# Kernel optimization log

Measured on AMD Instinct MI355X. Metric: run time of the kernel, lower is better.

## Reference

```python
import jax, jax.numpy as jnp
import numpy as np

D_MODEL = 1024
N_HEADS = 16
HEAD_DIM = D_MODEL // N_HEADS
B, T = 4, 2048


def setup_inputs() -> dict:
    key = jax.random.key(0)
    ks = jax.random.split(key, 5)
    s = 1.0 / np.sqrt(D_MODEL)
    return {
        "x": jax.random.normal(ks[0], (B, T, D_MODEL), dtype=jnp.float32),
        "Wq": jax.random.normal(ks[1], (D_MODEL, D_MODEL), dtype=jnp.float32) * s,
        "bq": jnp.zeros((D_MODEL,), jnp.float32),
        "Wk": jax.random.normal(ks[2], (D_MODEL, D_MODEL), dtype=jnp.float32) * s,
        "bk": jnp.zeros((D_MODEL,), jnp.float32),
        "Wv": jax.random.normal(ks[3], (D_MODEL, D_MODEL), dtype=jnp.float32) * s,
        "bv": jnp.zeros((D_MODEL,), jnp.float32),
        "Wo": jax.random.normal(ks[4], (D_MODEL, D_MODEL), dtype=jnp.float32) * s,
        "bo": jnp.zeros((D_MODEL,), jnp.float32),
    }


def reference(x, Wq, bq, Wk, bk, Wv, bv, Wo, bo):
    Bx, Tx, C = x.shape
    H, Dh = N_HEADS, HEAD_DIM
    # projections (torch Linear: y = x @ W.T + b)
    q = (x @ Wq.T + bq).reshape(Bx, Tx, H, Dh).transpose(0, 2, 1, 3)  # [B,H,T,Dh]
    k = (x @ Wk.T + bk).reshape(Bx, Tx, H, Dh).transpose(0, 2, 1, 3)
    v = (x @ Wv.T + bv).reshape(Bx, Tx, H, Dh).transpose(0, 2, 1, 3)
    scores = jnp.einsum("bhqd,bhkd->bhqk", q, k) / np.sqrt(Dh).astype(np.float32)
    causal = jnp.tril(jnp.ones((Tx, Tx), dtype=bool))
    scores = jnp.where(causal, scores, -jnp.inf)
    attn = jax.nn.softmax(scores, axis=-1)  # dropout in eval mode = identity
    y = jnp.einsum("bhqk,bhkd->bhqd", attn, v)
    y = y.transpose(0, 2, 1, 3).reshape(Bx, Tx, C)
    return y @ Wo.T + bo
```

## Files before the change

### kernel.cpp

```cpp
#include <hip/hip_runtime.h>

typedef __attribute__((ext_vector_type(8))) short short8;
typedef __attribute__((ext_vector_type(4))) float f32x4;
typedef unsigned short u16;
typedef unsigned int u32;

#define NH 16

#if __has_builtin(__builtin_amdgcn_exp2f)
#define EXP2(x) __builtin_amdgcn_exp2f(x)
#else
#define EXP2(x) exp2f(x)
#endif

__device__ __forceinline__ u32 f2bf(float f) {
  u32 u = __builtin_bit_cast(u32, f);
  return (u + 0x7fffu + ((u >> 16) & 1u)) >> 16;
}

__device__ __forceinline__ void gload_lds16(const u16* g, u16* l) {
  __builtin_amdgcn_global_load_lds(
      (const __attribute__((address_space(1))) void*)g,
      (__attribute__((address_space(3))) void*)l, 16, 0, 0);
}

__global__ __launch_bounds__(256) void k_convert(
    const float* __restrict__ x, const float* __restrict__ wq,
    const float* __restrict__ wk, const float* __restrict__ wv,
    const float* __restrict__ wo, u16* __restrict__ dst) {
  int i = blockIdx.x * 256 + threadIdx.x;
  size_t e = (size_t)i * 4;
  const float* s; size_t off;
  if (e < 8388608ull)       { s = x;  off = e; }
  else if (e < 9437184ull)  { s = wq; off = e - 8388608ull; }
  else if (e < 10485760ull) { s = wk; off = e - 9437184ull; }
  else if (e < 11534336ull) { s = wv; off = e - 10485760ull; }
  else                      { s = wo; off = e - 11534336ull; }
  float4 d = *(const float4*)(s + off);
  ushort4 o;
  o.x = (u16)f2bf(d.x); o.y = (u16)f2bf(d.y);
  o.z = (u16)f2bf(d.z); o.w = (u16)f2bf(d.w);
  *(ushort4*)(dst + e) = o;
}

#define GPHASE(MH, NH_, LA, LB)                                                \
  if (LA) {                                                                    \
    _Pragma("unroll")                                                          \
    for (int mt = 0; mt < 4; ++mt)                                             \
      _Pragma("unroll")                                                        \
      for (int ks = 0; ks < 2; ++ks)                                           \
        af[mt][ks] = *(const short8*)(Ab +                                     \
            (wr * MT * 16 + ((MH) * 4 + mt) * 16 + l16) * 64 +                 \
            ((ks * 4 + quad) ^ swz) * 8);                                      \
  }                                                                            \
  if (LB) {                                                                    \
    _Pragma("unroll")                                                          \
    for (int nt = 0; nt < NH2; ++nt)                                           \
      _Pragma("unroll")                                                        \
      for (int ks = 0; ks < 2; ++ks)                                           \
        bfr[nt][ks] = *(const short8*)(Bb +                                    \
            (wn * NT * 16 + ((NH_) * NH2 + nt) * 16 + l16) * 64 +              \
            ((ks * 4 + quad) ^ swz) * 8);                                      \
  }                                                                            \
  __builtin_amdgcn_s_barrier();                                                \
  __builtin_amdgcn_s_setprio(1);                                               \
  _Pragma("unroll")                                                            \
  for (int mt = 0; mt < 4; ++mt)                                               \
    _Pragma("unroll")                                                          \
    for (int nt = 0; nt < NH2; ++nt)                                           \
      _Pragma("unroll")                                                        \
      for (int ks = 0; ks < 2; ++ks)                                           \
        acc[(MH) * 4 + mt][(NH_) * NH2 + nt] =                                 \
            __builtin_amdgcn_mfma_f32_16x16x32_bf16(                           \
                af[mt][ks], bfr[nt][ks], acc[(MH) * 4 + mt][(NH_) * NH2 + nt], \
                0, 0, 0);                                                      \
  __builtin_amdgcn_s_setprio(0);                                               \
  __builtin_amdgcn_s_barrier();                                                \
  __builtin_amdgcn_sched_barrier(0);

#define STAGE_T(T, PB)                                                         \
  {                                                                            \
    const u16* aT = aTh + (T) * 64;                                            \
    const u16* bT = bTh + (T) * 64;                                            \
    u16* aD = &As[PB][0] + dbase;                                              \
    u16* bD = &Bs[PB][0] + dbase;                                              \
    _Pragma("unroll")                                                          \
    for (int j = 0; j < NLA; ++j) gload_lds16(aT + j * 65536, aD + j * 4096);  \
    _Pragma("unroll")                                                          \
    for (int j = 0; j < NLB; ++j) gload_lds16(bT + j * 65536, bD + j * 4096);  \
  }

template <int MT, int NT>
__device__ __forceinline__ void gemm_core(const u16* __restrict__ Aptr,
                                          const u16* __restrict__ Bptr,
                                          int m0, int n0, f32x4 (&acc)[8][4]) {
  constexpr int NLA = MT / 2;
  constexpr int NLB = NT;
  constexpr int NLD = NLA + NLB;
  constexpr int NH2 = NT / 2;
  __shared__ u16 As[2][MT * 32 * 64];
  __shared__ u16 Bs[2][NT * 64 * 64];
  const int tid = threadIdx.x;
  const int wave = tid >> 6, lane = tid & 63;
  const int quad = lane >> 4, l16 = lane & 15;
  const int wr = wave >> 2, wn = wave & 3;
  const int swz = l16 & 7;
  const int srow = tid >> 3;
  const int srcg = (tid & 7) ^ (srow & 7);
  const u16* aTh = Aptr + (size_t)(m0 + srow) * 1024 + srcg * 8;
  const u16* bTh = Bptr + (size_t)(n0 + srow) * 1024 + srcg * 8;
  const int dbase = wave * 512;

  {
    f32x4 z = {0.f, 0.f, 0.f, 0.f};
    #pragma unroll
    for (int a = 0; a < 8; ++a)
      #pragma unroll
      for (int b2 = 0; b2 < 4; ++b2) acc[a][b2] = z;
  }

  STAGE_T(0, 0)

  short8 af[4][2], bfr[NH2][2];
  for (int t = 0; t < 16; ++t) {
    const int p = t & 1;
    if (t < 15) {
      STAGE_T(t + 1, p ^ 1)
      if constexpr (NLD == 8)
        asm volatile("s_waitcnt vmcnt(8)" ::: "memory");
      else if constexpr (NLD == 6)
        asm volatile("s_waitcnt vmcnt(6)" ::: "memory");
      else
        asm volatile("s_waitcnt vmcnt(0)" ::: "memory");
    } else {
      asm volatile("s_waitcnt vmcnt(0)" ::: "memory");
    }
    __builtin_amdgcn_s_barrier();
    __builtin_amdgcn_sched_barrier(0);
    const u16* Ab = &As[p][0];
    const u16* Bb = &Bs[p][0];
    GPHASE(0, 0, true, true)
    GPHASE(0, 1, false, true)
    GPHASE(1, 1, true, false)
    GPHASE(1, 0, false, true)
  }
}

__global__ __launch_bounds__(512, 2) void k_gemm_qkv(
    const u16* __restrict__ A, const u16* __restrict__ W,
    const float* __restrict__ bq, const float* __restrict__ bk,
    const float* __restrict__ bv, u16* __restrict__ qkv,
    u16* __restrict__ vt) {
  const int bid = blockIdx.x;
  const int sw = (bid & 7) * 48 + (bid >> 3);
  const int ntile = sw % 12, mtile = sw / 12;
  const int m0 = mtile * 256, n0 = ntile * 256;
  const int z = n0 >> 10;
  const float* bias = (z == 0) ? bq : (z == 1) ? bk : bv;
  u16* out = qkv + (size_t)z * 8388608;
  const float scl = (z == 0) ? 0.125f * 1.44269504088896340736f : 1.0f;
  f32x4 acc[8][4];
  gemm_core<8, 4>(A, W, m0, n0, acc);
  const int tid = threadIdx.x;
  const int wave = tid >> 6, lane = tid & 63;
  const int quad = lane >> 4, l16 = lane & 15;
  const int wr = wave >> 2, wn = wave & 3;
  if (z == 2) {
    #pragma unroll
    for (int mt = 0; mt < 8; ++mt) {
      #pragma unroll
      for (int nt = 0; nt < 4; ++nt) {
        int nn = (n0 + wn * 64 + nt * 16 + l16) & 1023;
        float bn = bias[nn];
        int h = nn >> 6, d = nn & 63;
        int mbase = m0 + wr * 128 + mt * 16 + quad * 4;
        int b = mbase >> 11, tb = mbase & 2047;
        uint2 pk;
        pk.x = f2bf(acc[mt][nt][0] + bn) | (f2bf(acc[mt][nt][1] + bn) << 16);
        pk.y = f2bf(acc[mt][nt][2] + bn) | (f2bf(acc[mt][nt][3] + bn) << 16);
        *(uint2*)(vt + ((size_t)(b * NH + h) * 64 + d) * 2048 + tb) = pk;
      }
    }
  } else {
    #pragma unroll
    for (int mt = 0; mt < 8; ++mt) {
      #pragma unroll
      for (int nt = 0; nt < 4; ++nt) {
        int nn = (n0 + wn * 64 + nt * 16 + l16) & 1023;
        float bn = bias[nn];
        int h = nn >> 6, d = nn & 63;
        #pragma unroll
        for (int r = 0; r < 4; ++r) {
          int m = m0 + wr * 128 + mt * 16 + quad * 4 + r;
          int b = m >> 11, tt = m & 2047;
          float val = (acc[mt][nt][r] + bn) * scl;
          out[(((size_t)(b * NH + h) * 2048 + tt) << 6) + d] = (u16)f2bf(val);
        }
      }
    }
  }
}

__global__ __launch_bounds__(512, 2) void k_gemm_out(
    const u16* __restrict__ A, const u16* __restrict__ Bw,
    const float* __restrict__ bias, float* __restrict__ out) {
  const int bid = blockIdx.x;
  const int sw = (bid & 7) * 32 + (bid >> 3);
  const int mtile = sw >> 3, ntile = sw & 7;
  const int m0 = mtile * 256, n0 = ntile * 128;
  f32x4 acc[8][4];
  gemm_core<8, 2>(A, Bw, m0, n0, acc);
  const int tid = threadIdx.x;
  const int wave = tid >> 6, lane = tid & 63;
  const int quad = lane >> 4, l16 = lane & 15;
  const int wr = wave >> 2, wn = wave & 3;
  #pragma unroll
  for (int mt = 0; mt < 8; ++mt) {
    #pragma unroll
    for (int nt = 0; nt < 2; ++nt) {
      int n = n0 + wn * 32 + nt * 16 + l16;
      float bn = bias[n];
      #pragma unroll
      for (int r = 0; r < 4; ++r) {
        int m = m0 + wr * 128 + mt * 16 + quad * 4 + r;
        out[(size_t)m * 1024 + n] = acc[mt][nt][r] + bn;
      }
    }
  }
}

#define ATTN_SUB(P, QF0, QF1, O, MI, LI, DIAG)                                 \
  {                                                                            \
    f32x4 st[4];                                                               \
    _Pragma("unroll")                                                          \
    for (int nt = 0; nt < 4; ++nt) {                                           \
      short8 kf0 = *(const short8*)(&Ks[P][(nt * 16 + l16) * 72 + quad * 8]);  \
      short8 kf1 = *(const short8*)(&Ks[P][(nt * 16 + l16) * 72 + 32 + quad * 8]); \
      f32x4 z4 = {0.f, 0.f, 0.f, 0.f};                                         \
      z4 = __builtin_amdgcn_mfma_f32_16x16x32_bf16(kf0, QF0, z4, 0, 0, 0);     \
      st[nt] = __builtin_amdgcn_mfma_f32_16x16x32_bf16(kf1, QF1, z4, 0, 0, 0); \
    }                                                                          \
    if (DIAG) {                                                                \
      int q_loc = wave * 16 + l16;                                             \
      _Pragma("unroll")                                                        \
      for (int nt = 0; nt < 4; ++nt) {                                         \
        _Pragma("unroll")                                                      \
        for (int r = 0; r < 4; ++r) {                                          \
          int k_loc = nt * 16 + quad * 4 + r;                                  \
          if (k_loc > q_loc) st[nt][r] = -1e30f;                               \
        }                                                                      \
      }                                                                        \
    }                                                                          \
    float mq[4];                                                               \
    _Pragma("unroll")                                                          \
    for (int nt = 0; nt < 4; ++nt)                                             \
      mq[nt] = fmaxf(fmaxf(st[nt][0], st[nt][1]), fmaxf(st[nt][2], st[nt][3]));\
    float mx = fmaxf(fmaxf(mq[0], mq[1]), fmaxf(mq[2], mq[3]));                \
    mx = fmaxf(mx, __shfl_xor(mx, 16, 64));                                    \
    mx = fmaxf(mx, __shfl_xor(mx, 32, 64));                                    \
    float mnew = fmaxf(MI, mx);                                                \
    float alpha = EXP2(MI - mnew);                                             \
    MI = mnew;                                                                 \
    LI *= alpha;                                                               \
    _Pragma("unroll")                                                          \
    for (int r = 0; r < 4; ++r) {                                              \
      float av = __shfl(alpha, quad * 4 + r, 16);                              \
      _Pragma("unroll")                                                        \
      for (int dt = 0; dt < 4; ++dt) O[dt][r] *= av;                           \
    }                                                                          \
    u32 Wx[4], Wy[4];                                                          \
    float sq[4];                                                               \
    _Pragma("unroll")                                                          \
    for (int nt = 0; nt < 4; ++nt) {                                           \
      float p0 = EXP2(st[nt][0] - mnew);                                       \
      float p1 = EXP2(st[nt][1] - mnew);                                       \
      float p2 = EXP2(st[nt][2] - mnew);                                       \
      float p3 = EXP2(st[nt][3] - mnew);                                       \
      sq[nt] = (p0 + p1) + (p2 + p3);                                          \
      Wx[nt] = f2bf(p0) | (f2bf(p1) << 16);                                    \
      Wy[nt] = f2bf(p2) | (f2bf(p3) << 16);                                    \
    }                                                                          \
    float sum = (sq[0] + sq[1]) + (sq[2] + sq[3]);                             \
    sum += __shfl_xor(sum, 16, 64);                                            \
    sum += __shfl_xor(sum, 32, 64);                                            \
    LI += sum;                                                                 \
    uint4 t0, t1;                                                              \
    {                                                                          \
      u32 e, f;                                                                \
      e = __shfl(Wx[0], s0, 64); f = __shfl(Wx[1], s0, 64); t0.x = hi ? f : e; \
      e = __shfl(Wy[0], s0, 64); f = __shfl(Wy[1], s0, 64); t0.y = hi ? f : e; \
      e = __shfl(Wx[0], s1, 64); f = __shfl(Wx[1], s1, 64); t0.z = hi ? f : e; \
      e = __shfl(Wy[0], s1, 64); f = __shfl(Wy[1], s1, 64); t0.w = hi ? f : e; \
      e = __shfl(Wx[2], s0, 64); f = __shfl(Wx[3], s0, 64); t1.x = hi ? f : e; \
      e = __shfl(Wy[2], s0, 64); f = __shfl(Wy[3], s0, 64); t1.y = hi ? f : e; \
      e = __shfl(Wx[2], s1, 64); f = __shfl(Wx[3], s1, 64); t1.z = hi ? f : e; \
      e = __shfl(Wy[2], s1, 64); f = __shfl(Wy[3], s1, 64); t1.w = hi ? f : e; \
    }                                                                          \
    short8 pf0 = __builtin_bit_cast(short8, t0);                               \
    short8 pf1 = __builtin_bit_cast(short8, t1);                               \
    _Pragma("unroll")                                                          \
    for (int dt = 0; dt < 4; ++dt) {                                           \
      short8 vf0 = *(const short8*)(&Vs[P][(dt * 16 + l16) * 72 + quad * 8]);  \
      short8 vf1 = *(const short8*)(&Vs[P][(dt * 16 + l16) * 72 + 32 + quad * 8]); \
      O[dt] = __builtin_amdgcn_mfma_f32_16x16x32_bf16(pf0, vf0, O[dt], 0, 0, 0); \
      O[dt] = __builtin_amdgcn_mfma_f32_16x16x32_bf16(pf1, vf1, O[dt], 0, 0, 0); \
    }                                                                          \
  }

#define ATTN_EPI(O, LI, QT)                                                    \
  _Pragma("unroll")                                                            \
  for (int r = 0; r < 4; ++r) {                                                \
    float lv = __shfl(LI, quad * 4 + r, 16);                                   \
    float inv = 1.0f / lv;                                                     \
    int t = (QT) * 64 + wave * 16 + quad * 4 + r;                              \
    _Pragma("unroll")                                                          \
    for (int dt = 0; dt < 4; ++dt) {                                           \
      int d = dt * 16 + l16;                                                   \
      y[(((size_t)b * 2048 + t) * NH + h) * 64 + d] = (u16)f2bf(O[dt][r] * inv); \
    }                                                                          \
  }

__global__ __launch_bounds__(256, 4) void k_attn(
    const u16* __restrict__ q, const u16* __restrict__ k,
    const u16* __restrict__ vt, u16* __restrict__ y) {
  const int tid = threadIdx.x;
  const int wave = tid >> 6, lane = tid & 63;
  const int quad = lane >> 4, l16 = lane & 15;
  const int bh = blockIdx.x, bx = blockIdx.y;
  const int qtB = bx, qtA = 31 - bx;
  const int b = bh >> 4, h = bh & 15;

  __shared__ u16 Ks[2][64 * 72];
  __shared__ u16 Vs[2][64 * 72];

  const u16* qbA = q + ((size_t)bh * 2048 + qtA * 64 + wave * 16 + l16) * 64;
  short8 qA0 = *(const short8*)(qbA + quad * 8);
  short8 qA1 = *(const short8*)(qbA + 32 + quad * 8);
  const u16* qbB = q + ((size_t)bh * 2048 + qtB * 64 + wave * 16 + l16) * 64;
  short8 qB0 = *(const short8*)(qbB + quad * 8);
  short8 qB1 = *(const short8*)(qbB + 32 + quad * 8);

  f32x4 oA[4], oB[4];
  {
    f32x4 z = {0.f, 0.f, 0.f, 0.f};
    #pragma unroll
    for (int dt = 0; dt < 4; ++dt) { oA[dt] = z; oB[dt] = z; }
  }
  float mA = -1e30f, lA = 0.f, mB = -1e30f, lB = 0.f;

  const u16* kbase = k + (size_t)bh * 131072;
  const u16* vbase = vt + (size_t)bh * 131072;
  const int r0 = tid >> 3, cc = tid & 7;
  const int s0 = ((quad & 1) << 5) + l16, s1 = s0 + 16;
  const int hi = quad >> 1;

  {
    uint4 k0 = *(const uint4*)(kbase + (size_t)r0 * 64 + cc * 8);
    uint4 k1 = *(const uint4*)(kbase + (size_t)(r0 + 32) * 64 + cc * 8);
    uint4 v0 = *(const uint4*)(vbase + (size_t)r0 * 2048 + cc * 8);
    uint4 v1 = *(const uint4*)(vbase + (size_t)(r0 + 32) * 2048 + cc * 8);
    *(uint4*)(&Ks[0][r0 * 72 + cc * 8]) = k0;
    *(uint4*)(&Ks[0][(r0 + 32) * 72 + cc * 8]) = k1;
    *(uint4*)(&Vs[0][r0 * 72 + cc * 8]) = v0;
    *(uint4*)(&Vs[0][(r0 + 32) * 72 + cc * 8]) = v1;
  }
  __syncthreads();

  for (int kt = 0; kt <= qtA; ++kt) {
    const int p = kt & 1;
    const bool pre = (kt < qtA);
    uint4 kr0, kr1, vr0, vr1;
    if (pre) {
      const u16* kb = kbase + (size_t)(kt + 1) * 4096;
      const u16* vb = vbase + (kt + 1) * 64;
      kr0 = *(const uint4*)(kb + (size_t)r0 * 64 + cc * 8);
      kr1 = *(const uint4*)(kb + (size_t)(r0 + 32) * 64 + cc * 8);
      vr0 = *(const uint4*)(vb + (size_t)r0 * 2048 + cc * 8);
      vr1 = *(const uint4*)(vb + (size_t)(r0 + 32) * 2048 + cc * 8);
    }

    ATTN_SUB(p, qA0, qA1, oA, mA, lA, (kt == qtA))
    if (kt <= qtB) {
      ATTN_SUB(p, qB0, qB1, oB, mB, lB, (kt == qtB))
    }

    if (pre) {
      *(uint4*)(&Ks[p ^ 1][r0 * 72 + cc * 8]) = kr0;
      *(uint4*)(&Ks[p ^ 1][(r0 + 32) * 72 + cc * 8]) = kr1;
      *(uint4*)(&Vs[p ^ 1][r0 * 72 + cc * 8]) = vr0;
      *(uint4*)(&Vs[p ^ 1][(r0 + 32) * 72 + cc * 8]) = vr1;
    }
    __syncthreads();
  }

  ATTN_EPI(oA, lA, qtA)
  ATTN_EPI(oB, lB, qtB)
}

extern "C" void kernel_launch(void* const* d_in, const int* in_sizes, int n_in,
                              void* d_out, int out_size, void* d_ws, size_t ws_size,
                              hipStream_t stream) {
  const float* x  = (const float*)d_in[0];
  const float* Wq = (const float*)d_in[1];
  const float* bq = (const float*)d_in[2];
  const float* Wk = (const float*)d_in[3];
  const float* bk = (const float*)d_in[4];
  const float* Wv = (const float*)d_in[5];
  const float* bv = (const float*)d_in[6];
  const float* Wo = (const float*)d_in[7];
  const float* bo = (const float*)d_in[8];
  float* out = (float*)d_out;

  u16* ws  = (u16*)d_ws;
  u16* xb  = ws;
  u16* Wb  = ws + 8388608;
  u16* qkv = ws + 12582912;
  u16* vt  = ws + 37748736;
  u16* y   = ws + 46137344;

  k_convert<<<dim3(12288), dim3(256), 0, stream>>>(x, Wq, Wk, Wv, Wo, ws);
  k_gemm_qkv<<<dim3(384), dim3(512), 0, stream>>>(xb, Wb, bq, bk, bv, qkv, vt);
  k_attn<<<dim3(64, 16), dim3(256), 0, stream>>>(qkv, qkv + 8388608, vt, y);
  k_gemm_out<<<dim3(256), dim3(512), 0, stream>>>(y, Wb + 3 * 1048576, bo, out);
}
```

Baseline: 301.6 us.

## Halve QKV GEMM M-tile and use hardware packed bf16 conversion

The QKV projection GEMM now uses 128x256 tiles with 768 blocks instead of 256x256 with 384, so the grid covers the 256 CUs more evenly. The gemm core is generalized to the tile shape, with a matching vmcnt wait and a shortened phase sequence. Separately, software float-to-bf16 rounding in the convert, epilogue and attention softmax paths is replaced by the v_cvt_pk_bf16_f32 instruction. Smaller tiles lower data reuse and raise global and LDS traffic per flop. The hardware conversion may also differ slightly from the manual rounding on NaN handling.

```diff
diff --git a/kernel.cpp b/kernel.cpp
--- a/kernel.cpp
+++ b/kernel.cpp
@@ -16,6 +16,12 @@
 __device__ __forceinline__ u32 f2bf(float f) {
   u32 u = __builtin_bit_cast(u32, f);
   return (u + 0x7fffu + ((u >> 16) & 1u)) >> 16;
+}
+
+__device__ __forceinline__ u32 cvtpk(float lo, float hi) {
+  u32 r;
+  asm("v_cvt_pk_bf16_f32 %0, %1, %2" : "=v"(r) : "v"(lo), "v"(hi));
+  return r;
 }
 
 __device__ __forceinline__ void gload_lds16(const u16* g, u16* l) {
@@ -37,10 +43,10 @@
   else if (e < 11534336ull) { s = wv; off = e - 10485760ull; }
   else                      { s = wo; off = e - 11534336ull; }
   float4 d = *(const float4*)(s + off);
-  ushort4 o;
-  o.x = (u16)f2bf(d.x); o.y = (u16)f2bf(d.y);
-  o.z = (u16)f2bf(d.z); o.w = (u16)f2bf(d.w);
-  *(ushort4*)(dst + e) = o;
+  uint2 o;
+  o.x = cvtpk(d.x, d.y);
+  o.y = cvtpk(d.z, d.w);
+  *(uint2*)(dst + e) = o;
 }
 
 #define GPHASE(MH, NH_, LA, LB)                                                \
@@ -93,7 +99,8 @@
 template <int MT, int NT>
 __device__ __forceinline__ void gemm_core(const u16* __restrict__ Aptr,
                                           const u16* __restrict__ Bptr,
-                                          int m0, int n0, f32x4 (&acc)[8][4]) {
+                                          int m0, int n0,
+                                          f32x4 (&acc)[MT][NT]) {
   constexpr int NLA = MT / 2;
   constexpr int NLB = NT;
   constexpr int NLD = NLA + NLB;
@@ -114,9 +121,9 @@
   {
     f32x4 z = {0.f, 0.f, 0.f, 0.f};
     #pragma unroll
-    for (int a = 0; a < 8; ++a)
+    for (int a = 0; a < MT; ++a)
       #pragma unroll
-      for (int b2 = 0; b2 < 4; ++b2) acc[a][b2] = z;
+      for (int b2 = 0; b2 < NT; ++b2) acc[a][b2] = z;
   }
 
   STAGE_T(0, 0)
@@ -130,6 +137,8 @@
         asm volatile("s_waitcnt vmcnt(8)" ::: "memory");
       else if constexpr (NLD == 6)
         asm volatile("s_waitcnt vmcnt(6)" ::: "memory");
+      else if constexpr (NLD == 4)
+        asm volatile("s_waitcnt vmcnt(4)" ::: "memory");
       else
         asm volatile("s_waitcnt vmcnt(0)" ::: "memory");
     } else {
@@ -139,10 +148,15 @@
     __builtin_amdgcn_sched_barrier(0);
     const u16* Ab = &As[p][0];
     const u16* Bb = &Bs[p][0];
-    GPHASE(0, 0, true, true)
-    GPHASE(0, 1, false, true)
-    GPHASE(1, 1, true, false)
-    GPHASE(1, 0, false, true)
+    if constexpr (MT == 8) {
+      GPHASE(0, 0, true, true)
+      GPHASE(0, 1, false, true)
+      GPHASE(1, 1, true, false)
+      GPHASE(1, 0, false, true)
+    } else {
+      GPHASE(0, 0, true, true)
+      GPHASE(0, 1, false, true)
+    }
   }
 }
 
@@ -152,38 +166,38 @@
     const float* __restrict__ bv, u16* __restrict__ qkv,
     u16* __restrict__ vt) {
   const int bid = blockIdx.x;
-  const int sw = (bid & 7) * 48 + (bid >> 3);
-  const int ntile = sw % 12, mtile = sw / 12;
-  const int m0 = mtile * 256, n0 = ntile * 256;
+  const int xw = (bid & 7) * 96 + (bid >> 3);
+  const int mtile = xw / 12, ntile = xw % 12;
+  const int m0 = mtile * 128, n0 = ntile * 256;
   const int z = n0 >> 10;
   const float* bias = (z == 0) ? bq : (z == 1) ? bk : bv;
   u16* out = qkv + (size_t)z * 8388608;
   const float scl = (z == 0) ? 0.125f * 1.44269504088896340736f : 1.0f;
-  f32x4 acc[8][4];
-  gemm_core<8, 4>(A, W, m0, n0, acc);
+  f32x4 acc[4][4];
+  gemm_core<4, 4>(A, W, m0, n0, acc);
   const int tid = threadIdx.x;
   const int wave = tid >> 6, lane = tid & 63;
   const int quad = lane >> 4, l16 = lane & 15;
   const int wr = wave >> 2, wn = wave & 3;
   if (z == 2) {
     #pragma unroll
-    for (int mt = 0; mt < 8; ++mt) {
+    for (int mt = 0; mt < 4; ++mt) {
       #pragma unroll
       for (int nt = 0; nt < 4; ++nt) {
         int nn = (n0 + wn * 64 + nt * 16 + l16) & 1023;
         float bn = bias[nn];
         int h = nn >> 6, d = nn & 63;
-        int mbase = m0 + wr * 128 + mt * 16 + quad * 4;
+        int mbase = m0 + wr * 64 + mt * 16 + quad * 4;
         int b = mbase >> 11, tb = mbase & 2047;
         uint2 pk;
-        pk.x = f2bf(acc[mt][nt][0] + bn) | (f2bf(acc[mt][nt][1] + bn) << 16);
-        pk.y = f2bf(acc[mt][nt][2] + bn) | (f2bf(acc[mt][nt][3] + bn) << 16);
+        pk.x = cvtpk(acc[mt][nt][0] + bn, acc[mt][nt][1] + bn);
+        pk.y = cvtpk(acc[mt][nt][2] + bn, acc[mt][nt][3] + bn);
         *(uint2*)(vt + ((size_t)(b * NH + h) * 64 + d) * 2048 + tb) = pk;
       }
     }
   } else {
     #pragma unroll
-    for (int mt = 0; mt < 8; ++mt) {
+    for (int mt = 0; mt < 4; ++mt) {
       #pragma unroll
       for (int nt = 0; nt < 4; ++nt) {
         int nn = (n0 + wn * 64 + nt * 16 + l16) & 1023;
@@ -191,7 +205,7 @@
         int h = nn >> 6, d = nn & 63;
         #pragma unroll
         for (int r = 0; r < 4; ++r) {
-          int m = m0 + wr * 128 + mt * 16 + quad * 4 + r;
+          int m = m0 + wr * 64 + mt * 16 + quad * 4 + r;
           int b = m >> 11, tt = m & 2047;
           float val = (acc[mt][nt][r] + bn) * scl;
           out[(((size_t)(b * NH + h) * 2048 + tt) << 6) + d] = (u16)f2bf(val);
@@ -208,7 +222,7 @@
   const int sw = (bid & 7) * 32 + (bid >> 3);
   const int mtile = sw >> 3, ntile = sw & 7;
   const int m0 = mtile * 256, n0 = ntile * 128;
-  f32x4 acc[8][4];
+  f32x4 acc[8][2];
   gemm_core<8, 2>(A, Bw, m0, n0, acc);
   const int tid = threadIdx.x;
   const int wave = tid >> 6, lane = tid & 63;
@@ -277,8 +291,8 @@
       float p2 = EXP2(st[nt][2] - mnew);                                       \
       float p3 = EXP2(st[nt][3] - mnew);                                       \
       sq[nt] = (p0 + p1) + (p2 + p3);                                          \
-      Wx[nt] = f2bf(p0) | (f2bf(p1) << 16);                                    \
-      Wy[nt] = f2bf(p2) | (f2bf(p3) << 16);                                    \
+      Wx[nt] = cvtpk(p0, p1);                                                  \
+      Wy[nt] = cvtpk(p2, p3);                                                  \
     }                                                                          \
     float sum = (sq[0] + sq[1]) + (sq[2] + sq[3]);                             \
     sum += __shfl_xor(sum, 16, 64);                                            \
@@ -419,7 +433,7 @@
   u16* y   = ws + 46137344;
 
   k_convert<<<dim3(12288), dim3(256), 0, stream>>>(x, Wq, Wk, Wv, Wo, ws);
-  k_gemm_qkv<<<dim3(384), dim3(512), 0, stream>>>(xb, Wb, bq, bk, bv, qkv, vt);
+  k_gemm_qkv<<<dim3(768), dim3(512), 0, stream>>>(xb, Wb, bq, bk, bv, qkv, vt);
   k_attn<<<dim3(64, 16), dim3(256), 0, stream>>>(qkv, qkv + 8388608, vt, y);
   k_gemm_out<<<dim3(256), dim3(512), 0, stream>>>(y, Wb + 3 * 1048576, bo, out);
 }
```

After: 297.5 us. No clear change (-1.4%).
